# Kernel tuning notes

Measured on AMD Instinct MI355X. Metric: run time of the kernel, lower is better.

Reference implementation:

```python
import jax, jax.numpy as jnp
import numpy as np

K = 1024  # num_embeddings
D = 256   # embedding_dim
COMMIT = 0.25

def setup_inputs() -> dict:
    key = jax.random.key(0)
    k1, k2 = jax.random.split(key)
    z = jax.random.normal(k1, (32, 256, 32, 32), dtype=jnp.float32)
    # matches nn.Embedding init uniform_(-1/K, 1/K)
    emb = jax.random.uniform(k2, (K, D), dtype=jnp.float32, minval=-1.0 / K, maxval=1.0 / K)
    return {"z": z, "emb": emb}

def reference(z, emb):
    B, C, H, W = z.shape
    zp = jnp.transpose(z, (0, 2, 3, 1))            # (B,H,W,C)
    z_flat = zp.reshape(-1, C)                      # (N,D)
    # squared euclidean distances (N,K)
    d = (jnp.sum(z_flat * z_flat, axis=1, keepdims=True)
         + jnp.sum(emb * emb, axis=1)
         - 2.0 * z_flat @ emb.T)
    idx = jnp.argmin(d, axis=1)                     # (N,)
    quantized_flat = emb[idx]                       # gather == one-hot @ emb
    quantized = quantized_flat.reshape(zp.shape)    # (B,H,W,C)
    e_latent_loss = jnp.mean((jax.lax.stop_gradient(quantized) - zp) ** 2)
    q_latent_loss = jnp.mean((quantized - jax.lax.stop_gradient(zp)) ** 2)
    loss = q_latent_loss + COMMIT * e_latent_loss
    # straight-through estimator
    quantized_st = zp + jax.lax.stop_gradient(quantized - zp)
    # perplexity: avg one-hot probs == normalized counts
    N = z_flat.shape[0]
    counts = jnp.zeros((K,), dtype=jnp.float32).at[idx].add(1.0)
    avg_probs = counts / N
    perplexity = jnp.exp(-jnp.sum(avg_probs * jnp.log(avg_probs + 1e-10)))
    out = jnp.transpose(quantized_st, (0, 3, 1, 2))  # (B,C,H,W)
    return (out, loss, perplexity)
```

## Files before the change

### kernel.cpp

```cpp
#include <hip/hip_runtime.h>
#include <math.h>

#define KC 1024
#define DD 256
#define NROWS 32768
#define NELEM 8388608

typedef _Float16 f16;
typedef __attribute__((ext_vector_type(8))) _Float16 f16x8;
typedef __attribute__((ext_vector_type(16))) float f32x16;

#define KEY_SCALE 2097152.0f
#define KEY_INV   (1.0f / 2097152.0f)

__global__ void vq_prep_kernel(const float* __restrict__ emb, f16* __restrict__ emb_h,
                               float* __restrict__ c_sq, int* __restrict__ counts,
                               float* __restrict__ loss64, unsigned* __restrict__ done) {
    const int tid = threadIdx.x;
    const int gt = blockIdx.x * 256 + tid;
    if (gt < KC) counts[gt] = 0;
    if (gt < 64) loss64[gt] = 0.0f;
    if (gt == 0) *done = 0u;
    {
        int k = blockIdx.x * 4 + (tid >> 6);
        int lane = tid & 63;
        float4 v = *(const float4*)(emb + (size_t)k * DD + lane * 4);
        float s = v.x * v.x + v.y * v.y + v.z * v.z + v.w * v.w;
        #pragma unroll
        for (int off = 32; off > 0; off >>= 1) s += __shfl_down(s, off);
        if (lane == 0) c_sq[k] = s;
    }
    if (gt < 32768) {
        int code = gt & 1023;
        int kg = gt >> 10;
        const float* p = emb + (size_t)code * DD + kg * 8;
        float4 v0 = *(const float4*)p;
        float4 v1 = *(const float4*)(p + 4);
        f16x8 hcv;
        hcv[0] = (f16)v0.x; hcv[1] = (f16)v0.y; hcv[2] = (f16)v0.z; hcv[3] = (f16)v0.w;
        hcv[4] = (f16)v1.x; hcv[5] = (f16)v1.y; hcv[6] = (f16)v1.z; hcv[7] = (f16)v1.w;
        *(f16x8*)(emb_h + (size_t)gt * 8) = hcv;
    }
}

__global__ __launch_bounds__(512, 4)
void vq_argmin_kernel(const float* __restrict__ z, const f16* __restrict__ emb_h,
                      const float* __restrict__ c_sq, int* __restrict__ counts,
                      float* __restrict__ loss64, int* __restrict__ idx_g) {
    __shared__ __align__(16) f16 z_s[32 * 64 * 8];
    __shared__ int   bl_key[8][64];
    __shared__ float zsq_part[8][64];

    const int tid = threadIdx.x;
    const int n0 = blockIdx.x * 64;
    const int b = n0 >> 10;
    const int hw0 = n0 & 1023;

    ((int*)bl_key)[tid] = 0x7FFFFFFF;

    {
        const int r = tid & 63;
        const int kq = tid >> 6;
        const float* zp = z + (size_t)b * (DD * 1024) + hw0 + r;
        float sq = 0.f;
        #pragma unroll
        for (int it = 0; it < 4; ++it) {
            int kg = kq * 4 + it;
            f16x8 hv;
            #pragma unroll
            for (int j = 0; j < 8; ++j) {
                float v = zp[(size_t)(kg * 8 + j) * 1024];
                sq += v * v;
                hv[j] = (f16)v;
            }
            *(f16x8*)&z_s[(kg * 64 + r) * 8] = hv;
        }
        zsq_part[kq][r] = sq;
    }
    __syncthreads();

    const int m = tid & 31;
    const int h = (tid >> 5) & 1;
    const int w = tid >> 6;

    for (int p = 0; p < 2; ++p) {
        const int code0 = w * 128 + p * 64 + m;
        const int code1 = code0 + 32;
        const f16* eb0 = emb_h + (size_t)h * 8192 + (size_t)code0 * 8;
        const f16* eb1 = emb_h + (size_t)h * 8192 + (size_t)code1 * 8;

        f32x16 acc00, acc01, acc10, acc11;
        #pragma unroll
        for (int i = 0; i < 16; ++i) {
            acc00[i] = 0.f; acc01[i] = 0.f; acc10[i] = 0.f; acc11[i] = 0.f;
        }

        #pragma unroll 4
        for (int ks = 0; ks < 16; ++ks) {
            const f16* za = z_s + ((size_t)(2 * ks + h) * 64 + m) * 8;
            f16x8 a0 = *(const f16x8*)(za);
            f16x8 a1 = *(const f16x8*)(za + 256);
            f16x8 b0 = *(const f16x8*)(eb0 + (size_t)ks * 16384);
            f16x8 b1 = *(const f16x8*)(eb1 + (size_t)ks * 16384);
            acc00 = __builtin_amdgcn_mfma_f32_32x32x16_f16(a0, b0, acc00, 0, 0, 0);
            acc10 = __builtin_amdgcn_mfma_f32_32x32x16_f16(a1, b0, acc10, 0, 0, 0);
            acc01 = __builtin_amdgcn_mfma_f32_32x32x16_f16(a0, b1, acc01, 0, 0, 0);
            acc11 = __builtin_amdgcn_mfma_f32_32x32x16_f16(a1, b1, acc11, 0, 0, 0);
        }

        const float cs0 = c_sq[code0];
        const float cs1 = c_sq[code1];
        int bk0[16], bk1[16];
        #pragma unroll
        for (int reg = 0; reg < 16; ++reg) {
            float sA = fmaf(-2.f, acc00[reg], cs0);
            float sB = fmaf(-2.f, acc01[reg], cs1);
            int kA = (int)(sA * KEY_SCALE) * 1024 + code0;
            int kB = (int)(sB * KEY_SCALE) * 1024 + code1;
            bk0[reg] = min(kA, kB);
            sA = fmaf(-2.f, acc10[reg], cs0);
            sB = fmaf(-2.f, acc11[reg], cs1);
            kA = (int)(sA * KEY_SCALE) * 1024 + code0;
            kB = (int)(sB * KEY_SCALE) * 1024 + code1;
            bk1[reg] = min(kA, kB);
        }

        #pragma unroll
        for (int s = 0; s < 16; ++s) {
            int k0 = bk0[s], k1 = bk1[s];
            #pragma unroll
            for (int d = 16; d >= 1; d >>= 1) {
                k0 = min(k0, __shfl_xor(k0, d));
                k1 = min(k1, __shfl_xor(k1, d));
            }
            bk0[s] = k0; bk1[s] = k1;
        }
        if (m == 0) {
            #pragma unroll
            for (int s = 0; s < 16; ++s) {
                int row = (s & 3) + 8 * (s >> 2) + 4 * h;
                bl_key[w][row]      = min(bl_key[w][row],      bk0[s]);
                bl_key[w][32 + row] = min(bl_key[w][32 + row], bk1[s]);
            }
        }
    }
    __syncthreads();

    if (tid < 64) {
        int k = bl_key[0][tid];
        #pragma unroll
        for (int w2 = 1; w2 < 8; ++w2) k = min(k, bl_key[w2][tid]);
        int i = k & 1023;
        idx_g[n0 + tid] = i;
        atomicAdd(&counts[i], 1);
        float zq = 0.f;
        #pragma unroll
        for (int p2 = 0; p2 < 8; ++p2) zq += zsq_part[p2][tid];
        float lr = (float)(k >> 10) * KEY_INV + zq;
        #pragma unroll
        for (int off = 32; off > 0; off >>= 1) lr += __shfl_down(lr, off);
        if (tid == 0) atomicAdd(&loss64[blockIdx.x & 63], lr);
    }
}

__global__ __launch_bounds__(512, 4)
void vq_out_kernel(const float* __restrict__ emb, const int* __restrict__ idx_g,
                   const int* __restrict__ counts, const float* __restrict__ loss64,
                   unsigned* __restrict__ done, float* __restrict__ out,
                   float* __restrict__ out_tail) {
    __shared__ __align__(16) float Qh[32 * 260];
    __shared__ int   idx_s[64];
    __shared__ float wsum[8];
    __shared__ int   flag_s;

    const int tid = threadIdx.x;
    const int n0 = blockIdx.x * 64;
    const int b = n0 >> 10;
    const int hw0 = n0 & 1023;

    if (tid < 64) idx_s[tid] = idx_g[n0 + tid];
    __syncthreads();

    #pragma unroll
    for (int hh = 0; hh < 2; ++hh) {
        {
            int r = tid & 31;
            int part = tid >> 5;
            const float* ep = emb + (size_t)idx_s[hh * 32 + r] * DD + part * 16;
            float* qrow = Qh + r * 260 + part * 16;
            #pragma unroll
            for (int g = 0; g < 4; ++g)
                *(float4*)(qrow + g * 4) = *(const float4*)(ep + g * 4);
        }
        __syncthreads();
        {
            int r = tid & 31;
            int part = tid >> 5;
            const float* qr = Qh + r * 260;
            const size_t base = (size_t)b * (DD * 1024) + hw0 + hh * 32 + r;
            #pragma unroll
            for (int g = 0; g < 4; ++g) {
                int c0 = part * 16 + g * 4;
                float4 v = *(const float4*)(qr + c0);
                out[base + (size_t)c0 * 1024] = v.x;
                out[base + (size_t)(c0 + 1) * 1024] = v.y;
                out[base + (size_t)(c0 + 2) * 1024] = v.z;
                out[base + (size_t)(c0 + 3) * 1024] = v.w;
            }
        }
        __syncthreads();
    }

    if (tid == 0) {
        __threadfence();
        flag_s = (atomicAdd(done, 1u) == 511u) ? 1 : 0;
    }
    __syncthreads();
    if (flag_s) {
        float s = 0.f;
        for (int k = tid; k < KC; k += 512) {
            float pr = (float)counts[k] * (1.0f / (float)NROWS);
            s += pr * logf(pr + 1e-10f);
        }
        #pragma unroll
        for (int off = 32; off > 0; off >>= 1) s += __shfl_down(s, off);
        if ((tid & 63) == 0) wsum[tid >> 6] = s;
        __syncthreads();
        float loss_tot = 0.f;
        if (tid < 64) {
            float lv = loss64[tid];
            #pragma unroll
            for (int off = 32; off > 0; off >>= 1) lv += __shfl_down(lv, off);
            loss_tot = lv;
        }
        if (tid == 0) {
            float ent = 0.f;
            #pragma unroll
            for (int p = 0; p < 8; ++p) ent += wsum[p];
            out_tail[0] = 1.25f * loss_tot * (1.0f / (float)NELEM);
            out_tail[1] = expf(-ent);
        }
    }
}

extern "C" void kernel_launch(void* const* d_in, const int* in_sizes, int n_in,
                              void* d_out, int out_size, void* d_ws, size_t ws_size,
                              hipStream_t stream) {
    const float* z = (const float*)d_in[0];
    const float* emb = (const float*)d_in[1];
    float* out = (float*)d_out;

    char* wsb = (char*)d_ws;
    f16* emb_h = (f16*)wsb;
    float* c_sq = (float*)(wsb + 524288);
    int* counts = (int*)(wsb + 528384);
    float* loss64 = (float*)(wsb + 532480);
    unsigned* done = (unsigned*)(wsb + 532736);
    int* idx_g = (int*)(wsb + 535040);

    hipLaunchKernelGGL(vq_prep_kernel, dim3(256), dim3(256), 0, stream,
                       emb, emb_h, c_sq, counts, loss64, done);
    hipLaunchKernelGGL(vq_argmin_kernel, dim3(512), dim3(512), 0, stream,
                       z, emb_h, c_sq, counts, loss64, idx_g);
    hipLaunchKernelGGL(vq_out_kernel, dim3(512), dim3(512), 0, stream,
                       emb, idx_g, counts, loss64, done, out, out + NELEM);
}
```

Measured before the change: 139.1 us.

## Double argmin block threads and split output kernel across channel halves

```diff
diff --git a/kernel.cpp b/kernel.cpp
--- a/kernel.cpp
+++ b/kernel.cpp
@@ -43,13 +43,13 @@
     }
 }
 
-__global__ __launch_bounds__(512, 4)
+__global__ __launch_bounds__(1024, 8)
 void vq_argmin_kernel(const float* __restrict__ z, const f16* __restrict__ emb_h,
                       const float* __restrict__ c_sq, int* __restrict__ counts,
                       float* __restrict__ loss64, int* __restrict__ idx_g) {
     __shared__ __align__(16) f16 z_s[32 * 64 * 8];
-    __shared__ int   bl_key[8][64];
-    __shared__ float zsq_part[8][64];
+    __shared__ int   bl_key[16][64];
+    __shared__ float zsq_part[16][64];
 
     const int tid = threadIdx.x;
     const int n0 = blockIdx.x * 64;
@@ -64,8 +64,8 @@
         const float* zp = z + (size_t)b * (DD * 1024) + hw0 + r;
         float sq = 0.f;
         #pragma unroll
-        for (int it = 0; it < 4; ++it) {
-            int kg = kq * 4 + it;
+        for (int it = 0; it < 2; ++it) {
+            int kg = kq * 2 + it;
             f16x8 hv;
             #pragma unroll
             for (int j = 0; j < 8; ++j) {
@@ -83,46 +83,32 @@
     const int h = (tid >> 5) & 1;
     const int w = tid >> 6;
 
-    for (int p = 0; p < 2; ++p) {
-        const int code0 = w * 128 + p * 64 + m;
-        const int code1 = code0 + 32;
-        const f16* eb0 = emb_h + (size_t)h * 8192 + (size_t)code0 * 8;
-        const f16* eb1 = emb_h + (size_t)h * 8192 + (size_t)code1 * 8;
-
-        f32x16 acc00, acc01, acc10, acc11;
-        #pragma unroll
-        for (int i = 0; i < 16; ++i) {
-            acc00[i] = 0.f; acc01[i] = 0.f; acc10[i] = 0.f; acc11[i] = 0.f;
-        }
-
-        #pragma unroll 4
+    for (int c = 0; c < 2; ++c) {
+        const int code = w * 64 + c * 32 + m;
+        const f16* ebp = emb_h + (size_t)h * 8192 + (size_t)code * 8;
+
+        f32x16 acc0, acc1;
+        #pragma unroll
+        for (int i = 0; i < 16; ++i) { acc0[i] = 0.f; acc1[i] = 0.f; }
+
+        #pragma unroll 2
         for (int ks = 0; ks < 16; ++ks) {
             const f16* za = z_s + ((size_t)(2 * ks + h) * 64 + m) * 8;
             f16x8 a0 = *(const f16x8*)(za);
             f16x8 a1 = *(const f16x8*)(za + 256);
-            f16x8 b0 = *(const f16x8*)(eb0 + (size_t)ks * 16384);
-            f16x8 b1 = *(const f16x8*)(eb1 + (size_t)ks * 16384);
-            acc00 = __builtin_amdgcn_mfma_f32_32x32x16_f16(a0, b0, acc00, 0, 0, 0);
-            acc10 = __builtin_amdgcn_mfma_f32_32x32x16_f16(a1, b0, acc10, 0, 0, 0);
-            acc01 = __builtin_amdgcn_mfma_f32_32x32x16_f16(a0, b1, acc01, 0, 0, 0);
-            acc11 = __builtin_amdgcn_mfma_f32_32x32x16_f16(a1, b1, acc11, 0, 0, 0);
-        }
-
-        const float cs0 = c_sq[code0];
-        const float cs1 = c_sq[code1];
+            f16x8 b0 = *(const f16x8*)(ebp + (size_t)ks * 16384);
+            acc0 = __builtin_amdgcn_mfma_f32_32x32x16_f16(a0, b0, acc0, 0, 0, 0);
+            acc1 = __builtin_amdgcn_mfma_f32_32x32x16_f16(a1, b0, acc1, 0, 0, 0);
+        }
+
+        const float cs = c_sq[code];
         int bk0[16], bk1[16];
         #pragma unroll
         for (int reg = 0; reg < 16; ++reg) {
-            float sA = fmaf(-2.f, acc00[reg], cs0);
-            float sB = fmaf(-2.f, acc01[reg], cs1);
-            int kA = (int)(sA * KEY_SCALE) * 1024 + code0;
-            int kB = (int)(sB * KEY_SCALE) * 1024 + code1;
-            bk0[reg] = min(kA, kB);
-            sA = fmaf(-2.f, acc10[reg], cs0);
-            sB = fmaf(-2.f, acc11[reg], cs1);
-            kA = (int)(sA * KEY_SCALE) * 1024 + code0;
-            kB = (int)(sB * KEY_SCALE) * 1024 + code1;
-            bk1[reg] = min(kA, kB);
+            float s0 = fmaf(-2.f, acc0[reg], cs);
+            float s1 = fmaf(-2.f, acc1[reg], cs);
+            bk0[reg] = (int)(s0 * KEY_SCALE) * 1024 + code;
+            bk1[reg] = (int)(s1 * KEY_SCALE) * 1024 + code;
         }
 
         #pragma unroll
@@ -149,13 +135,13 @@
     if (tid < 64) {
         int k = bl_key[0][tid];
         #pragma unroll
-        for (int w2 = 1; w2 < 8; ++w2) k = min(k, bl_key[w2][tid]);
+        for (int w2 = 1; w2 < 16; ++w2) k = min(k, bl_key[w2][tid]);
         int i = k & 1023;
         idx_g[n0 + tid] = i;
         atomicAdd(&counts[i], 1);
         float zq = 0.f;
         #pragma unroll
-        for (int p2 = 0; p2 < 8; ++p2) zq += zsq_part[p2][tid];
+        for (int p2 = 0; p2 < 16; ++p2) zq += zsq_part[p2][tid];
         float lr = (float)(k >> 10) * KEY_INV + zq;
         #pragma unroll
         for (int off = 32; off > 0; off >>= 1) lr += __shfl_down(lr, off);
@@ -163,57 +149,56 @@
     }
 }
 
-__global__ __launch_bounds__(512, 4)
+__global__ __launch_bounds__(512, 8)
 void vq_out_kernel(const float* __restrict__ emb, const int* __restrict__ idx_g,
                    const int* __restrict__ counts, const float* __restrict__ loss64,
                    unsigned* __restrict__ done, float* __restrict__ out,
                    float* __restrict__ out_tail) {
-    __shared__ __align__(16) float Qh[32 * 260];
+    __shared__ float Qt[128][65];
     __shared__ int   idx_s[64];
     __shared__ float wsum[8];
     __shared__ int   flag_s;
 
     const int tid = threadIdx.x;
-    const int n0 = blockIdx.x * 64;
+    const int tile = blockIdx.x >> 1;
+    const int ch0 = (blockIdx.x & 1) * 128;
+    const int n0 = tile * 64;
     const int b = n0 >> 10;
     const int hw0 = n0 & 1023;
 
     if (tid < 64) idx_s[tid] = idx_g[n0 + tid];
     __syncthreads();
 
-    #pragma unroll
-    for (int hh = 0; hh < 2; ++hh) {
-        {
-            int r = tid & 31;
-            int part = tid >> 5;
-            const float* ep = emb + (size_t)idx_s[hh * 32 + r] * DD + part * 16;
-            float* qrow = Qh + r * 260 + part * 16;
-            #pragma unroll
-            for (int g = 0; g < 4; ++g)
-                *(float4*)(qrow + g * 4) = *(const float4*)(ep + g * 4);
-        }
-        __syncthreads();
-        {
-            int r = tid & 31;
-            int part = tid >> 5;
-            const float* qr = Qh + r * 260;
-            const size_t base = (size_t)b * (DD * 1024) + hw0 + hh * 32 + r;
-            #pragma unroll
-            for (int g = 0; g < 4; ++g) {
-                int c0 = part * 16 + g * 4;
-                float4 v = *(const float4*)(qr + c0);
-                out[base + (size_t)c0 * 1024] = v.x;
-                out[base + (size_t)(c0 + 1) * 1024] = v.y;
-                out[base + (size_t)(c0 + 2) * 1024] = v.z;
-                out[base + (size_t)(c0 + 3) * 1024] = v.w;
-            }
-        }
-        __syncthreads();
+    {
+        int r = tid & 63;
+        int p = tid >> 6;
+        const float* ep = emb + (size_t)idx_s[r] * DD + ch0 + p * 16;
+        float4 v0 = *(const float4*)(ep);
+        float4 v1 = *(const float4*)(ep + 4);
+        float4 v2 = *(const float4*)(ep + 8);
+        float4 v3 = *(const float4*)(ep + 12);
+        float vv[16] = {v0.x, v0.y, v0.z, v0.w, v1.x, v1.y, v1.z, v1.w,
+                        v2.x, v2.y, v2.z, v2.w, v3.x, v3.y, v3.z, v3.w};
+        #pragma unroll
+        for (int g = 0; g < 16; ++g)
+            Qt[p * 16 + g][r] = vv[g];
+    }
+    __syncthreads();
+
+    {
+        int lane = tid & 63;
+        int w = tid >> 6;
+        const size_t base = (size_t)b * (DD * 1024) + hw0 + lane;
+        #pragma unroll
+        for (int g = 0; g < 16; ++g) {
+            int ch = w * 16 + g;
+            out[base + (size_t)(ch0 + ch) * 1024] = Qt[ch][lane];
+        }
     }
 
     if (tid == 0) {
         __threadfence();
-        flag_s = (atomicAdd(done, 1u) == 511u) ? 1 : 0;
+        flag_s = (atomicAdd(done, 1u) == 1023u) ? 1 : 0;
     }
     __syncthreads();
     if (flag_s) {
@@ -260,8 +245,8 @@
 
     hipLaunchKernelGGL(vq_prep_kernel, dim3(256), dim3(256), 0, stream,
                        emb, emb_h, c_sq, counts, loss64, done);
-    hipLaunchKernelGGL(vq_argmin_kernel, dim3(512), dim3(512), 0, stream,
+    hipLaunchKernelGGL(vq_argmin_kernel, dim3(512), dim3(1024), 0, stream,
                        z, emb_h, c_sq, counts, loss64, idx_g);
-    hipLaunchKernelGGL(vq_out_kernel, dim3(512), dim3(512), 0, stream,
+    hipLaunchKernelGGL(vq_out_kernel, dim3(1024), dim3(512), 0, stream,
                        emb, idx_g, counts, loss64, done, out, out + NELEM);
 }
```

Result: slower. 177.2 us (+27.4%).
